# Performance work log

Measured on AMD Instinct MI355X. Metric: run time of the kernel, lower is better.

The kernel has to match this reference:

```python
import jax, jax.numpy as jnp
import numpy as np


def setup_inputs() -> dict:
    key = jax.random.key(0)
    ks = jax.random.split(key, 9)
    bs, d, K, h = 2048, 128, 256, 256
    s = 0.02  # weight init scale
    return {
        "xhat": jax.random.normal(ks[0], (bs, d), jnp.float32),
        "x": jax.random.normal(ks[1], (bs, d), jnp.float32),
        "codebook": jax.random.normal(ks[2], (K, d), jnp.float32),
        "Wc": jax.random.normal(ks[3], (d, 2 * d), jnp.float32) * s,
        "bc": jnp.zeros((d,), jnp.float32),
        "W1_0": jax.random.normal(ks[4], (h, d), jnp.float32) * s,
        "W2_0": jax.random.normal(ks[5], (d, h), jnp.float32) * s,
        "W1_1": jax.random.normal(ks[6], (h, d), jnp.float32) * s,
        "W2_1": jax.random.normal(ks[7], (d, h), jnp.float32) * s,
    }


def reference(xhat, x, codebook, Wc, bc, W1_0, W2_0, W1_1, W2_1):
    # QINCoStep.encode: evaluate all K codebook candidates per batch element.
    d = xhat.shape[1]
    # MLPconcat on concat([zqs, xhat], -1): split Wc [d, 2d] into codebook and xhat parts,
    # so we never materialize the (bs*K, 2d) concatenated tensor.
    Wz, Wx = Wc[:, :d], Wc[:, d:]
    z = (codebook + codebook @ Wz.T)[None, :, :] + (xhat @ Wx.T)[:, None, :] + bc  # [bs, K, d]
    for W1, W2 in ((W1_0, W2_0), (W1_1, W2_1)):
        z = z + jax.nn.relu(jnp.einsum("bkd,hd->bkh", z, W1)) @ W2.T
    cand = z + xhat[:, None, :]  # [bs, K, d] candidate reconstructions
    dist = jnp.sum(jnp.square(cand - x[:, None, :]), axis=-1)  # [bs, K]
    codes = jnp.argmin(dist, axis=1)  # [bs]
    xhat_next = jnp.take_along_axis(cand, codes[:, None, None], axis=1)[:, 0]  # [bs, d]
    return codes, xhat_next - xhat
```

## Files before the change

### kernel.cpp

```cpp
#include <hip/hip_runtime.h>


typedef short bf8_t __attribute__((ext_vector_type(8)));
typedef float f32x16 __attribute__((ext_vector_type(16)));

__device__ inline unsigned short f2bh(float x) {
    unsigned u = __float_as_uint(x);
    u += 0x7fffu + ((u >> 16) & 1u);
    return (unsigned short)(u >> 16);
}
__device__ inline float bh2f(unsigned short h) {
    return __uint_as_float(((unsigned)h) << 16);
}
__device__ inline f32x16 mfma_bf(uint4 a, uint4 b, f32x16 c) {
    bf8_t av = __builtin_bit_cast(bf8_t, a);
    bf8_t bv = __builtin_bit_cast(bf8_t, b);
    return __builtin_amdgcn_mfma_f32_32x32x16_bf16(av, bv, c, 0, 0, 0);
}
__device__ inline unsigned packhi(float x, float y) {
    return __builtin_amdgcn_perm(__float_as_uint(y), __float_as_uint(x), 0x07060302u);
}
__device__ inline unsigned addrelu2t(unsigned hv, unsigned uv) {
    float a0 = __uint_as_float(hv << 16) + __uint_as_float(uv << 16);
    float a1 = __uint_as_float(hv & 0xFFFF0000u) + __uint_as_float(uv & 0xFFFF0000u);
    return packhi(fmaxf(a0, 0.f), fmaxf(a1, 0.f));
}

#define DELTA 6.5f

__global__ __launch_bounds__(256) void k_prep1(
    const float* __restrict__ Wc,
    const float* __restrict__ W1a, const float* __restrict__ W2a,
    const float* __restrict__ W1b, const float* __restrict__ W2b,
    float* __restrict__ WzT, float* __restrict__ WxT,
    float* __restrict__ W1Ta, float* __restrict__ W2Ta,
    float* __restrict__ W1Tb, float* __restrict__ W2Tb,
    uint4* __restrict__ F)
{
    int g = blockIdx.x * 256 + threadIdx.x;
    if (g < 16384) {
        int j = g >> 7, d = g & 127;
        WzT[g] = Wc[d * 256 + j];
    } else if (g < 32768) {
        int e = g - 16384; int j = e >> 7, d = e & 127;
        WxT[e] = Wc[d * 256 + 128 + j];
    } else if (g < 65536) {
        int e = g - 32768; int d = e >> 8, h = e & 255;
        W1Ta[e] = W1a[h * 128 + d];
    } else if (g < 98304) {
        int e = g - 65536; int h = e >> 7, i = e & 127;
        W2Ta[e] = W2a[i * 256 + h];
    } else if (g < 131072) {
        int e = g - 98304; int d = e >> 8, h = e & 255;
        W1Tb[e] = W1b[h * 128 + d];
    } else if (g < 163840) {
        int e = g - 131072; int h = e >> 7, i = e & 127;
        W2Tb[e] = W2b[i * 256 + h];
    } else if (g < 176128) {
        int idx = g - 163840;
        int mat = idx >> 12, fp = idx & 4095;
        int tile = fp >> 6, lane = fp & 63;
        const float* src;
        if (mat == 1) {
            int mt = tile >> 3, kt = tile & 7;
            src = W1b + (32 * mt + (lane & 31)) * 128 + 16 * kt + 8 * (lane >> 5);
        } else {
            const float* W = (mat == 0) ? W2a : W2b;
            int mt = tile >> 4, kt = tile & 15;
            src = W + (32 * mt + (lane & 31)) * 256 + 16 * kt + 8 * (lane >> 5);
        }
        unsigned short hs[8];
#pragma unroll
        for (int j = 0; j < 8; ++j) hs[j] = f2bh(src[j]);
        uint4 hv;
        hv.x = (unsigned)hs[0] | ((unsigned)hs[1] << 16);
        hv.y = (unsigned)hs[2] | ((unsigned)hs[3] << 16);
        hv.z = (unsigned)hs[4] | ((unsigned)hs[5] << 16);
        hv.w = (unsigned)hs[6] | ((unsigned)hs[7] << 16);
        F[idx] = hv;
    }
}

__global__ __launch_bounds__(256) void k_prep2(
    const float* __restrict__ cb, const float* __restrict__ bc,
    const float* __restrict__ xhat,
    const float* __restrict__ WzT, const float* __restrict__ WxT,
    const float* __restrict__ W1T0,
    float* __restrict__ z0, unsigned short* __restrict__ z0bf,
    unsigned short* __restrict__ H1bf,
    float* __restrict__ u, unsigned short* __restrict__ ubf,
    unsigned short* __restrict__ U1bf)
{
    __shared__ float src[4][128];
    __shared__ float res[4][128];
    const int t = threadIdx.x;
    const bool krole = blockIdx.x < 64;
    const int r0 = (krole ? blockIdx.x : (blockIdx.x - 64)) * 4;
    const float* in = krole ? cb : xhat;
    const float* WT = krole ? WzT : WxT;
#pragma unroll
    for (int e = t; e < 512; e += 256)
        src[e >> 7][e & 127] = in[(r0 + (e >> 7)) * 128 + (e & 127)];
    __syncthreads();
    {
        const int d = t & 127, r = t >> 7;
        float a0 = krole ? (bc[d] + src[r][d]) : 0.f;
        float a1 = krole ? (bc[d] + src[r + 2][d]) : 0.f;
        for (int j = 0; j < 128; ++j) {
            const float w = WT[j * 128 + d];
            a0 = fmaf(src[r][j], w, a0);
            a1 = fmaf(src[r + 2][j], w, a1);
        }
        float* dst = krole ? z0 : u;
        unsigned short* dstbf = krole ? z0bf : ubf;
        dst[(r0 + r) * 128 + d] = a0;        dstbf[(r0 + r) * 128 + d] = f2bh(a0);
        dst[(r0 + r + 2) * 128 + d] = a1;    dstbf[(r0 + r + 2) * 128 + d] = f2bh(a1);
        res[r][d] = a0; res[r + 2][d] = a1;
    }
    __syncthreads();
    {
        float a[4] = {0.f, 0.f, 0.f, 0.f};
        for (int d = 0; d < 128; ++d) {
            const float w = W1T0[d * 256 + t];
#pragma unroll
            for (int r = 0; r < 4; ++r) a[r] = fmaf(res[r][d], w, a[r]);
        }
        if (krole) {
            const int kt = t >> 4, half = (t >> 3) & 1, j = t & 7;
#pragma unroll
            for (int r = 0; r < 4; ++r) {
                int k = r0 + r; int kg = k >> 5, col = k & 31;
                H1bf[(((kg * 16 + kt) * 64) + half * 32 + col) * 8 + j] = f2bh(a[r]);
            }
        } else {
#pragma unroll
            for (int r = 0; r < 4; ++r)
                U1bf[(r0 + r) * 256 + t] = f2bh(a[r]);
        }
    }
}

__global__ __launch_bounds__(512, 6) void k_dist_approx(
    const unsigned short* __restrict__ z0bf, const unsigned short* __restrict__ ubf,
    const float* __restrict__ xhat, const float* __restrict__ x,
    const uint4* __restrict__ H1u4, const unsigned short* __restrict__ U1bf,
    const uint4* __restrict__ W2f0, const uint4* __restrict__ W1f1,
    const uint4* __restrict__ W2f1,
    int* __restrict__ cand, int* __restrict__ cnt)
{
    __shared__ uint4 Zf[2048];
    __shared__ uint4 Hf[1024];

    const int t = threadIdx.x;
    const int lane = t & 63, wave = t >> 6;
    const int wm = wave & 3, wn = wave >> 2;
    const int l31 = lane & 31, l5 = lane >> 5;
    const int b = blockIdx.x >> 1, q = blockIdx.x & 1;
    const int k0 = q << 7;

    f32x16 zs[2];
    {
        const unsigned short* ur = ubf + b * 128;
#pragma unroll
        for (int g = 0; g < 2; ++g) {
            const int col = ((wn << 1) + g) * 32 + l31;
            const unsigned short* zr = z0bf + (k0 + col) * 128;
#pragma unroll
            for (int rg = 0; rg < 4; ++rg) {
                const int d0 = 32 * wm + 8 * rg + 4 * l5;
                ushort4 a = *(const ushort4*)(zr + d0);
                ushort4 c = *(const ushort4*)(ur + d0);
                zs[g][4*rg+0] = bh2f(a.x) + bh2f(c.x);
                zs[g][4*rg+1] = bh2f(a.y) + bh2f(c.y);
                zs[g][4*rg+2] = bh2f(a.z) + bh2f(c.z);
                zs[g][4*rg+3] = bh2f(a.w) + bh2f(c.w);
            }
        }
    }

#pragma unroll 1
    for (int r = 0; r < 4; ++r) {
        {
            const int kt = 4 * r + wm;
            const uint4 uv = *(const uint4*)(U1bf + b * 256 + kt * 16 + 8 * l5);
#pragma unroll
            for (int gi = 0; gi < 2; ++gi) {
                const int cg = (wn << 1) + gi;
                const int kg = (q << 2) + cg;
                uint4 hv = H1u4[(kg * 16 + kt) * 64 + lane];
                uint4 o;
                o.x = addrelu2t(hv.x, uv.x);
                o.y = addrelu2t(hv.y, uv.y);
                o.z = addrelu2t(hv.z, uv.z);
                o.w = addrelu2t(hv.w, uv.w);
                Hf[((cg << 2) + wm) * 64 + lane] = o;
            }
        }
        __syncthreads();
#pragma unroll
        for (int ktl = 0; ktl < 4; ++ktl) {
            uint4 ah = W2f0[((wm << 4) + 4 * r + ktl) * 64 + lane];
#pragma unroll
            for (int g = 0; g < 2; ++g) {
                uint4 bv = Hf[((((wn << 1) + g) << 2) + ktl) * 64 + lane];
                zs[g] = mfma_bf(ah, bv, zs[g]);
            }
        }
        __syncthreads();
    }

#pragma unroll
    for (int g = 0; g < 2; ++g) {
        const int cg = (wn << 1) + g;
#pragma unroll
        for (int rg = 0; rg < 4; ++rg) {
            uint2 hv;
            hv.x = packhi(zs[g][4*rg+0], zs[g][4*rg+1]);
            hv.y = packhi(zs[g][4*rg+2], zs[g][4*rg+3]);
            uint2* zb2 = (uint2*)&Zf[((cg << 3) + 2 * wm + (rg >> 1)) * 64];
            zb2[(((rg & 1) << 5) + l31) * 2 + l5] = hv;
        }
    }
    __syncthreads();

    const int tile = wave & 1, cg1 = wave >> 1;
#pragma unroll 1
    for (int c = 0; c < 4; ++c) {
        f32x16 acc;
#pragma unroll
        for (int rr = 0; rr < 16; ++rr) acc[rr] = 0.f;
        {
            const uint4* pw1 = W1f1 + ((2 * c + tile) << 3) * 64;
#pragma unroll
            for (int kt = 0; kt < 8; ++kt) {
                uint4 bv = Zf[((cg1 << 3) + kt) * 64 + lane];
                uint4 ah = pw1[kt * 64 + lane];
                acc = mfma_bf(ah, bv, acc);
            }
        }
        __syncthreads();
#pragma unroll
        for (int rg = 0; rg < 4; ++rg) {
            float v0 = fmaxf(acc[4*rg+0], 0.f), v1 = fmaxf(acc[4*rg+1], 0.f);
            float v2 = fmaxf(acc[4*rg+2], 0.f), v3 = fmaxf(acc[4*rg+3], 0.f);
            uint2 hv; hv.x = packhi(v0, v1); hv.y = packhi(v2, v3);
            uint2* hb2 = (uint2*)&Hf[((cg1 << 2) + (tile << 1) + (rg >> 1)) * 64];
            hb2[(((rg & 1) << 5) + l31) * 2 + l5] = hv;
        }
        __syncthreads();
#pragma unroll
        for (int ktl = 0; ktl < 4; ++ktl) {
            uint4 ah = W2f1[((wm << 4) + 4 * c + ktl) * 64 + lane];
#pragma unroll
            for (int g = 0; g < 2; ++g) {
                uint4 bv = Hf[((((wn << 1) + g) << 2) + ktl) * 64 + lane];
                zs[g] = mfma_bf(ah, bv, zs[g]);
            }
        }
    }

    float* red   = (float*)Hf;
    float* sdist = (float*)Hf + 512;
    int*   sk    = (int*)((float*)Hf + 640);
    __syncthreads();
#pragma unroll
    for (int g = 0; g < 2; ++g) {
        float s = 0.f;
        const int col = ((wn << 1) + g) * 32 + l31;
#pragma unroll
        for (int rg = 0; rg < 4; ++rg) {
            const int d0 = 32 * wm + 8 * rg + 4 * l5;
            float4 xh = *(const float4*)(xhat + b * 128 + d0);
            float4 xx = *(const float4*)(x + b * 128 + d0);
            float v;
            v = zs[g][4*rg+0] + xh.x - xx.x; s = fmaf(v, v, s);
            v = zs[g][4*rg+1] + xh.y - xx.y; s = fmaf(v, v, s);
            v = zs[g][4*rg+2] + xh.z - xx.z; s = fmaf(v, v, s);
            v = zs[g][4*rg+3] + xh.w - xx.w; s = fmaf(v, v, s);
        }
        s += __shfl_xor(s, 32, 64);
        if (l5 == 0) red[wm * 128 + col] = s;
    }
    __syncthreads();
    if (t < 128)
        sdist[t] = red[t] + red[128 + t] + red[256 + t] + red[384 + t];
    __syncthreads();
    if (wave == 0) {
        int base = 0;
        float v0 = sdist[lane], v1 = sdist[lane + 64];
        float m = fminf(v0, v1);
#pragma unroll
        for (int off = 32; off > 0; off >>= 1) m = fminf(m, __shfl_xor(m, off, 64));
        const float thr = m + DELTA;
        const unsigned long long below = (1ull << lane) - 1;
        float vv[2] = {v0, v1};
#pragma unroll
        for (int j = 0; j < 2; ++j) {
            bool p = vv[j] <= thr;
            unsigned long long mask = __ballot(p);
            int pos = base + __popcll(mask & below);
            if (p && pos < 8) sk[pos] = k0 + 64 * j + lane;
            base += __popcll(mask);
        }
        if (lane == 0) {
            int c = base > 8 ? 8 : base;
            cnt[b * 2 + q] = c;
            for (int s2 = 0; s2 < c; ++s2)
                cand[(b * 2 + q) * 8 + s2] = sk[s2];
        }
    }
}

__global__ __launch_bounds__(256) void k_final2(
    const float* __restrict__ z0, const float* __restrict__ u,
    const float* __restrict__ xhat, const float* __restrict__ x,
    const int* __restrict__ cand, const int* __restrict__ cnt,
    const float* __restrict__ W1Ta, const float* __restrict__ W2Ta,
    const float* __restrict__ W1Tb, const float* __restrict__ W2Tb,
    float* __restrict__ out0, float* __restrict__ outd)
{
    __shared__ float z16[16][128];
    __shared__ float h8[8][256];
    __shared__ int ck[16];
    __shared__ float dd[16];
    __shared__ int widx;
    const int t = threadIdx.x, b = blockIdx.x;
    const int c0 = cnt[2 * b], c1 = cnt[2 * b + 1];
    const int tot = c0 + c1;
    if (t < 16) {
        int k;
        if (t < c0)          k = cand[2 * b * 8 + t];
        else if (t < tot)    k = cand[(2 * b + 1) * 8 + (t - c0)];
        else                 k = cand[2 * b * 8];
        ck[t] = k;
    }
    __syncthreads();
    const int nb = (tot > 8) ? 2 : 1;
#pragma unroll 1
    for (int batch = 0; batch < nb; ++batch) {
        const int bo = batch * 8;
        const float* ub = u + b * 128;
#pragma unroll
        for (int n = 0; n < 4; ++n) {
            int e = n * 256 + t; int r = e >> 7, d = e & 127;
            z16[bo + r][d] = z0[ck[bo + r] * 128 + d] + ub[d];
        }
        __syncthreads();
        const float* W1T = W1Ta; const float* W2T = W2Ta;
#pragma unroll 1
        for (int blk = 0; blk < 2; ++blk) {
            float a1[8] = {0.f,0.f,0.f,0.f,0.f,0.f,0.f,0.f};
            for (int d = 0; d < 128; ++d) {
                const float w = W1T[d * 256 + t];
#pragma unroll
                for (int r = 0; r < 8; ++r) a1[r] = fmaf(z16[bo + r][d], w, a1[r]);
            }
#pragma unroll
            for (int r = 0; r < 8; ++r) h8[r][t] = fmaxf(a1[r], 0.f);
            __syncthreads();
            const int ig = t & 127, rg = (t >> 7) * 4;
            float a2[4] = {0.f,0.f,0.f,0.f};
            for (int h = 0; h < 256; ++h) {
                const float w = W2T[h * 128 + ig];
#pragma unroll
                for (int j = 0; j < 4; ++j) a2[j] = fmaf(h8[rg + j][h], w, a2[j]);
            }
            __syncthreads();
#pragma unroll
            for (int j = 0; j < 4; ++j) z16[bo + rg + j][ig] += a2[j];
            __syncthreads();
            W1T = W1Tb; W2T = W2Tb;
        }
        {
            float* part = (float*)h8;
            const int r = t >> 5, c = t & 31;
            float s = 0.f;
#pragma unroll
            for (int i = 0; i < 4; ++i) {
                int d = c * 4 + i;
                float v = z16[bo + r][d] + xhat[b * 128 + d] - x[b * 128 + d];
                s = fmaf(v, v, s);
            }
            part[r * 32 + c] = s;
            __syncthreads();
            if (t < 8) {
                float ssum = 0.f;
#pragma unroll
                for (int c2 = 0; c2 < 32; ++c2) ssum += part[t * 32 + c2];
                dd[bo + t] = ssum;
            }
            __syncthreads();
        }
    }
    if (t == 0) {
        float bv = dd[0]; int w = 0;
        for (int s = 1; s < tot; ++s)
            if (dd[s] < bv) { bv = dd[s]; w = s; }
        widx = w;
        out0[b] = (float)ck[w];
    }
    __syncthreads();
    if (t < 128) outd[b * 128 + t] = z16[widx][t];
}

extern "C" void kernel_launch(void* const* d_in, const int* in_sizes, int n_in,
                              void* d_out, int out_size, void* d_ws, size_t ws_size,
                              hipStream_t stream) {
    const float* xhat = (const float*)d_in[0];
    const float* x    = (const float*)d_in[1];
    const float* cb   = (const float*)d_in[2];
    const float* Wc   = (const float*)d_in[3];
    const float* bc   = (const float*)d_in[4];
    const float* W1_0 = (const float*)d_in[5];
    const float* W2_0 = (const float*)d_in[6];
    const float* W1_1 = (const float*)d_in[7];
    const float* W2_1 = (const float*)d_in[8];
    float* out = (float*)d_out;
    float* ws  = (float*)d_ws;

    float* WzT   = ws + 0;
    float* WxT   = ws + 16384;
    float* W1T0  = ws + 32768;
    float* W2T0  = ws + 65536;
    float* W1T1  = ws + 98304;
    float* W2T1  = ws + 131072;
    float* z0    = ws + 163840;
    float* u     = ws + 196608;
    unsigned short* z0bf = (unsigned short*)(ws + 458752);
    unsigned short* ubf  = (unsigned short*)(ws + 475136);
    unsigned short* U1bf = (unsigned short*)(ws + 606208);
    unsigned short* H1bf = (unsigned short*)(ws + 868352);
    uint4* F     = (uint4*)(ws + 901120);
    const uint4* W2f0 = F;
    const uint4* W1f1 = F + 4096;
    const uint4* W2f1 = F + 8192;
    int* cand = (int*)(ws + 950272);
    int* cnt  = (int*)(ws + 983040);

    k_prep1<<<688, 256, 0, stream>>>(Wc, W1_0, W2_0, W1_1, W2_1,
                                     WzT, WxT, W1T0, W2T0, W1T1, W2T1, F);
    k_prep2<<<576, 256, 0, stream>>>(cb, bc, xhat, WzT, WxT, W1T0,
                                     z0, z0bf, H1bf, u, ubf, U1bf);
    k_dist_approx<<<4096, 512, 0, stream>>>(z0bf, ubf, xhat, x, (const uint4*)H1bf,
                                            U1bf, W2f0, W1f1, W2f1, cand, cnt);
    k_final2<<<2048, 256, 0, stream>>>(z0, u, xhat, x, cand, cnt,
                                       W1T0, W2T0, W1T1, W2T1, out, out + 2048);
}
```

Measured before the change: 339.9 us.

## Pack candidate rows from eight batch elements into shared 16-row refinement tiles

The final exact-refinement kernel now handles eight batch elements per block. It builds a compacted list of all their candidate rows and processes them in 16-row tiles through the fp32 MLP, keeping a running best per element. This removes the half-empty 8-row tiles and the per-element reload of the MLP weights, so each weight load is reused across more rows. In exchange the block count drops from 2048 to 256, which lowers occupancy on a large GPU, and the kernel adds serial bookkeeping for prefix offsets and best-row tracking.

Result: slower. 456.8 us (+34.4%).

```diff
diff --git a/kernel.cpp b/kernel.cpp
--- a/kernel.cpp
+++ b/kernel.cpp
@@ -311,7 +311,7 @@
     }
 }
 
-__global__ __launch_bounds__(256) void k_final2(
+__global__ __launch_bounds__(256) void k_final3(
     const float* __restrict__ z0, const float* __restrict__ u,
     const float* __restrict__ xhat, const float* __restrict__ x,
     const int* __restrict__ cand, const int* __restrict__ cnt,
@@ -320,87 +320,130 @@
     float* __restrict__ out0, float* __restrict__ outd)
 {
     __shared__ float z16[16][128];
-    __shared__ float h8[8][256];
-    __shared__ int ck[16];
+    __shared__ float h16[16][256];
+    __shared__ float zwin[8][128];
+    __shared__ int rowb[128], rowk[128];
+    __shared__ int off[8];
+    __shared__ int rtot;
     __shared__ float dd[16];
-    __shared__ int widx;
-    const int t = threadIdx.x, b = blockIdx.x;
-    const int c0 = cnt[2 * b], c1 = cnt[2 * b + 1];
-    const int tot = c0 + c1;
-    if (t < 16) {
-        int k;
-        if (t < c0)          k = cand[2 * b * 8 + t];
-        else if (t < tot)    k = cand[(2 * b + 1) * 8 + (t - c0)];
-        else                 k = cand[2 * b * 8];
-        ck[t] = k;
-    }
-    __syncthreads();
-    const int nb = (tot > 8) ? 2 : 1;
+    __shared__ float dbest[8];
+    __shared__ int kbest[8];
+    __shared__ int copyrow[8];
+    const int t = threadIdx.x;
+    const int b0 = blockIdx.x * 8;
+
+    if (t < 8) {
+        int c0 = cnt[2 * (b0 + t)], c1 = cnt[2 * (b0 + t) + 1];
+        int tb = c0 + c1;
+        off[t] = tb;
+        dbest[t] = 3.4e38f;
+        kbest[t] = 0;
+    }
+    __syncthreads();
+    if (t == 0) {
+        int a = 0;
+        for (int i = 0; i < 8; ++i) { int v = off[i]; off[i] = a; a += v; }
+        rtot = a;
+    }
+    __syncthreads();
+    if (t < 8) {
+        int c0 = cnt[2 * (b0 + t)], c1 = cnt[2 * (b0 + t) + 1];
+        int o = off[t];
+        for (int s = 0; s < c0; ++s) { rowb[o] = t; rowk[o] = cand[(2 * (b0 + t)) * 8 + s]; ++o; }
+        for (int s = 0; s < c1; ++s) { rowb[o] = t; rowk[o] = cand[(2 * (b0 + t) + 1) * 8 + s]; ++o; }
+    }
+    __syncthreads();
+    const int R = rtot;
+    const int nb = (R + 15) >> 4;
+
 #pragma unroll 1
     for (int batch = 0; batch < nb; ++batch) {
-        const int bo = batch * 8;
-        const float* ub = u + b * 128;
-#pragma unroll
-        for (int n = 0; n < 4; ++n) {
+        const int rb0 = batch * 16;
+        const int nr = (R - rb0) < 16 ? (R - rb0) : 16;
+#pragma unroll
+        for (int n = 0; n < 8; ++n) {
             int e = n * 256 + t; int r = e >> 7, d = e & 127;
-            z16[bo + r][d] = z0[ck[bo + r] * 128 + d] + ub[d];
+            int rg = rb0 + (r < nr ? r : 0);
+            z16[r][d] = z0[rowk[rg] * 128 + d] + u[(b0 + rowb[rg]) * 128 + d];
         }
         __syncthreads();
         const float* W1T = W1Ta; const float* W2T = W2Ta;
 #pragma unroll 1
         for (int blk = 0; blk < 2; ++blk) {
-            float a1[8] = {0.f,0.f,0.f,0.f,0.f,0.f,0.f,0.f};
+            float a1[16];
+#pragma unroll
+            for (int r = 0; r < 16; ++r) a1[r] = 0.f;
             for (int d = 0; d < 128; ++d) {
                 const float w = W1T[d * 256 + t];
 #pragma unroll
-                for (int r = 0; r < 8; ++r) a1[r] = fmaf(z16[bo + r][d], w, a1[r]);
-            }
-#pragma unroll
-            for (int r = 0; r < 8; ++r) h8[r][t] = fmaxf(a1[r], 0.f);
+                for (int r = 0; r < 16; ++r) a1[r] = fmaf(z16[r][d], w, a1[r]);
+            }
+#pragma unroll
+            for (int r = 0; r < 16; ++r) h16[r][t] = fmaxf(a1[r], 0.f);
             __syncthreads();
-            const int ig = t & 127, rg = (t >> 7) * 4;
-            float a2[4] = {0.f,0.f,0.f,0.f};
+            const int ig = t & 127, rq = (t >> 7) * 8;
+            float a2[8];
+#pragma unroll
+            for (int j = 0; j < 8; ++j) a2[j] = 0.f;
             for (int h = 0; h < 256; ++h) {
                 const float w = W2T[h * 128 + ig];
 #pragma unroll
-                for (int j = 0; j < 4; ++j) a2[j] = fmaf(h8[rg + j][h], w, a2[j]);
+                for (int j = 0; j < 8; ++j) a2[j] = fmaf(h16[rq + j][h], w, a2[j]);
             }
             __syncthreads();
 #pragma unroll
-            for (int j = 0; j < 4; ++j) z16[bo + rg + j][ig] += a2[j];
+            for (int j = 0; j < 8; ++j) z16[rq + j][ig] += a2[j];
             __syncthreads();
             W1T = W1Tb; W2T = W2Tb;
         }
         {
-            float* part = (float*)h8;
-            const int r = t >> 5, c = t & 31;
+            float* part = (float*)h16;
+            const int r = t >> 4, c = t & 15;
+            const int bl = rowb[rb0 + (r < nr ? r : 0)];
             float s = 0.f;
 #pragma unroll
-            for (int i = 0; i < 4; ++i) {
-                int d = c * 4 + i;
-                float v = z16[bo + r][d] + xhat[b * 128 + d] - x[b * 128 + d];
+            for (int i = 0; i < 8; ++i) {
+                int d = c * 8 + i;
+                float v = z16[r][d] + xhat[(b0 + bl) * 128 + d] - x[(b0 + bl) * 128 + d];
                 s = fmaf(v, v, s);
             }
-            part[r * 32 + c] = s;
+            part[r * 16 + c] = s;
             __syncthreads();
-            if (t < 8) {
+            if (t < 16) {
                 float ssum = 0.f;
 #pragma unroll
-                for (int c2 = 0; c2 < 32; ++c2) ssum += part[t * 32 + c2];
-                dd[bo + t] = ssum;
-            }
-            __syncthreads();
-        }
-    }
-    if (t == 0) {
-        float bv = dd[0]; int w = 0;
-        for (int s = 1; s < tot; ++s)
-            if (dd[s] < bv) { bv = dd[s]; w = s; }
-        widx = w;
-        out0[b] = (float)ck[w];
-    }
-    __syncthreads();
-    if (t < 128) outd[b * 128 + t] = z16[widx][t];
+                for (int c2 = 0; c2 < 16; ++c2) ssum += part[t * 16 + c2];
+                dd[t] = ssum;
+            }
+        }
+        if (t < 8) copyrow[t] = -1;
+        __syncthreads();
+        if (t < 8) {
+            for (int r = 0; r < nr; ++r) {
+                if (rowb[rb0 + r] == t && dd[r] < dbest[t]) {
+                    dbest[t] = dd[r];
+                    kbest[t] = rowk[rb0 + r];
+                    copyrow[t] = r;
+                }
+            }
+        }
+        __syncthreads();
+        if (t < 128) {
+#pragma unroll 1
+            for (int bl = 0; bl < 8; ++bl) {
+                int cr = copyrow[bl];
+                if (cr >= 0) zwin[bl][t] = z16[cr][t];
+            }
+        }
+        __syncthreads();
+    }
+
+    if (t < 8) out0[b0 + t] = (float)kbest[t];
+#pragma unroll
+    for (int n = 0; n < 4; ++n) {
+        int e = n * 256 + t; int bl = e >> 7, d = e & 127;
+        outd[(b0 + bl) * 128 + d] = zwin[bl][d];
+    }
 }
 
 extern "C" void kernel_launch(void* const* d_in, const int* in_sizes, int n_in,
@@ -443,6 +486,6 @@
                                      z0, z0bf, H1bf, u, ubf, U1bf);
     k_dist_approx<<<4096, 512, 0, stream>>>(z0bf, ubf, xhat, x, (const uint4*)H1bf,
                                             U1bf, W2f0, W1f1, W2f1, cand, cnt);
-    k_final2<<<2048, 256, 0, stream>>>(z0, u, xhat, x, cand, cnt,
-                                       W1T0, W2T0, W1T1, W2T1, out, out + 2048);
-}
+    k_final3<<<256, 256, 0, stream>>>(z0, u, xhat, x, cand, cnt,
+                                      W1T0, W2T0, W1T1, W2T1, out, out + 2048);
+}
```
